# Optimization experiments

Measured on AMD Instinct MI355X. Metric: run time of the kernel, lower is better.

Reference implementation:

```python
import jax, jax.numpy as jnp
import numpy as np

EPS = 1e-5

def layer_norm(x, gamma, beta):
    mu = jnp.mean(x, axis=-1, keepdims=True)
    var = jnp.mean(jnp.square(x - mu), axis=-1, keepdims=True)
    return (x - mu) * jax.lax.rsqrt(var + EPS) * gamma + beta

def setup_inputs() -> dict:
    key = jax.random.key(0)
    ks = jax.random.split(key, 16)
    B, Cq, Hq, Wq = 8, 256, 32, 32
    Cc, Hc, Wc = 512, 64, 64
    def lin(k, fan_in, fan_out):
        lim = 1.0 / np.sqrt(fan_in)
        k1, k2 = jax.random.split(k)
        W = jax.random.uniform(k1, (fan_in, fan_out), jnp.float32, -lim, lim)
        b = jax.random.uniform(k2, (fan_out,), jnp.float32, -lim, lim)
        return W, b
    Wq_, bq = lin(ks[0], Cq, Cq)
    Wk_, bk = lin(ks[1], Cc, Cq)
    Wv_, bv = lin(ks[2], Cc, Cq)
    Wo_, bo = lin(ks[3], Cq, Cq)
    return {
        "query": jax.random.normal(ks[4], (B, Cq, Hq, Wq), jnp.float32),
        "context": jax.random.normal(ks[5], (B, Cc, Hc, Wc), jnp.float32),
        "Wq": Wq_, "bq": bq, "Wk": Wk_, "bk": bk, "Wv": Wv_, "bv": bv,
        "Wo": Wo_, "bo": bo,
        "gq": jnp.ones((Cq,), jnp.float32), "betq": jnp.zeros((Cq,), jnp.float32),
        "gc": jnp.ones((Cc,), jnp.float32), "betc": jnp.zeros((Cc,), jnp.float32),
    }

def reference(query, context, Wq, bq, Wk, bk, Wv, bv, Wo, bo, gq, betq, gc, betc):
    B, Cq, Hq, Wq_sp = query.shape
    _, Cc, Hc, Wc = context.shape
    num_heads = 8
    head_dim = Cq // num_heads
    scale = jnp.sqrt(jnp.float32(head_dim))
    N = Hq * Wq_sp
    # adaptive_avg_pool2d with divisible sizes == average pooling over equal bins
    ctx = context.reshape(B, Cc, Hq, Hc // Hq, Wq_sp, Wc // Wq_sp).mean(axis=(3, 5))
    q_flat = query.reshape(B, Cq, N).transpose(0, 2, 1)          # (B,N,Cq)
    c_flat = ctx.reshape(B, Cc, N).transpose(0, 2, 1)            # (B,N,Cc)
    qn = layer_norm(q_flat, gq, betq)
    cn = layer_norm(c_flat, gc, betc)
    q = (qn @ Wq + bq).reshape(B, N, num_heads, head_dim).transpose(0, 2, 1, 3)
    k = (cn @ Wk + bk).reshape(B, N, num_heads, head_dim).transpose(0, 2, 1, 3)
    v = (cn @ Wv + bv).reshape(B, N, num_heads, head_dim).transpose(0, 2, 1, 3)
    attn = jnp.einsum('bhnd,bhmd->bhnm', q, k) / scale
    attn = jax.nn.softmax(attn, axis=-1)
    out = jnp.einsum('bhnm,bhmd->bhnd', attn, v)
    out = out.transpose(0, 2, 1, 3).reshape(B, N, Cq)
    out = out @ Wo + bo
    out = q_flat + out                                           # residual
    return out.transpose(0, 2, 1).reshape(B, Cq, Hq, Wq_sp)
```

## Files before the change

### kernel.cpp

```cpp
#include <hip/hip_runtime.h>
#include <hip/hip_bf16.h>
#include <cstddef>

#define B_  8
#define CQ  256
#define CC  512
#define N_  1024
#define HQ  32
#define WQ  32
#define NH  8
#define HD  32

typedef __bf16 bf16x8 __attribute__((ext_vector_type(8)));
typedef float f32x4 __attribute__((ext_vector_type(4)));
typedef float f32x16 __attribute__((ext_vector_type(16)));
typedef unsigned int uint4v __attribute__((ext_vector_type(4)));
typedef unsigned short ushort8 __attribute__((ext_vector_type(8)));
typedef unsigned short ushort4v __attribute__((ext_vector_type(4)));

__device__ __forceinline__ unsigned short f2bf(float x) {
    return __builtin_bit_cast(unsigned short, __float2bfloat16(x));
}
__device__ __forceinline__ float bf2f(unsigned short x) {
    return __bfloat162float(__builtin_bit_cast(__hip_bfloat16, x));
}
__device__ __forceinline__ bf16x8 ldb8(const unsigned short* p) {
    return __builtin_bit_cast(bf16x8, *(const ushort8*)p);
}

__global__ __launch_bounds__(256) void prep_k(
    const float* __restrict__ query, const float* __restrict__ context,
    const float* __restrict__ Wq, const float* __restrict__ Wk,
    const float* __restrict__ Wv, const float* __restrict__ Wo,
    const float* __restrict__ gq, const float* __restrict__ betq,
    const float* __restrict__ gc, const float* __restrict__ betc,
    __hip_bfloat16* __restrict__ Wqt, __hip_bfloat16* __restrict__ Wkt,
    __hip_bfloat16* __restrict__ Wvt, __hip_bfloat16* __restrict__ Wot,
    __hip_bfloat16* __restrict__ qn, __hip_bfloat16* __restrict__ cn,
    __hip_bfloat16* __restrict__ qraw) {
    __shared__ float T[32][33];
    __shared__ float SsA[32][16];
    __shared__ float S2A[32][16];
    __shared__ float SsB[32][32];
    __shared__ float S2B[32][32];
    __shared__ float Mu[32], Rs[32];

    const int bid = blockIdx.x;
    const int tid = threadIdx.x;

    if (bid < 256) {
        const int nt = bid & 31, b = bid >> 5;
        const int nq = tid & 7;
        const int cg = tid >> 3;
        const int ch0 = cg * 8;
        const int nb  = nt * 32 + 4 * nq;

        const float* Qb = query + ((size_t)b * CQ + ch0) * N_ + nb;
        float qv[32];
        float ps[4] = {0.f, 0.f, 0.f, 0.f};
        float p2[4] = {0.f, 0.f, 0.f, 0.f};
        #pragma unroll
        for (int i = 0; i < 8; ++i) {
            const float4 v = *(const float4*)(Qb + (size_t)i * N_);
            qv[4 * i + 0] = v.x; qv[4 * i + 1] = v.y;
            qv[4 * i + 2] = v.z; qv[4 * i + 3] = v.w;
            ps[0] += v.x; p2[0] += v.x * v.x;
            ps[1] += v.y; p2[1] += v.y * v.y;
            ps[2] += v.z; p2[2] += v.z * v.z;
            ps[3] += v.w; p2[3] += v.w * v.w;
        }
        #pragma unroll
        for (int i = 0; i < 8; ++i) {
            ushort4v o;
            o[0] = f2bf(qv[4 * i + 0]); o[1] = f2bf(qv[4 * i + 1]);
            o[2] = f2bf(qv[4 * i + 2]); o[3] = f2bf(qv[4 * i + 3]);
            *(ushort4v*)((unsigned short*)qraw + ((size_t)b * CQ + ch0 + i) * N_ + nb) = o;
        }
        #pragma unroll
        for (int j = 0; j < 4; ++j) {
            SsB[cg][4 * nq + j] = ps[j];
            S2B[cg][4 * nq + j] = p2[j];
        }
        __syncthreads();
        if (tid < 32) {
            float ts = 0.f, t2 = 0.f;
            #pragma unroll
            for (int i = 0; i < 32; ++i) { ts += SsB[i][tid]; t2 += S2B[i][tid]; }
            const float mu  = ts * (1.f / CQ);
            const float var = t2 * (1.f / CQ) - mu * mu;
            Mu[tid] = mu; Rs[tid] = rsqrtf(var + 1e-5f);
        }
        __syncthreads();
        #pragma unroll
        for (int j = 0; j < 4; ++j) {
            const float mu = Mu[4 * nq + j], rs = Rs[4 * nq + j];
            ushort8 o;
            #pragma unroll
            for (int i = 0; i < 8; ++i)
                o[i] = f2bf((qv[4 * i + j] - mu) * rs * gq[ch0 + i] + betq[ch0 + i]);
            *(ushort8*)((unsigned short*)qn + ((size_t)b * N_ + nb + j) * CQ + ch0) = o;
        }
    } else if (bid < 768) {
        const int u    = bid - 256;
        const int wqc2 = u & 1, hq = (u >> 1) & 31, b = u >> 6;
        const int pp   = tid & 7;
        const int cg   = tid >> 3;
        const int ch0  = cg * 16;

        const float* Cb = context + ((size_t)b * CC + ch0) * 4096
                        + (size_t)(2 * hq) * 64 + (32 * wqc2 + 4 * pp);
        float pv0[16], pv1[16];
        float ss0 = 0.f, ss1 = 0.f, s20 = 0.f, s21 = 0.f;
        #pragma unroll
        for (int i = 0; i < 16; ++i) {
            const float4 r0 = *(const float4*)(Cb + (size_t)i * 4096);
            const float4 r1 = *(const float4*)(Cb + (size_t)i * 4096 + 64);
            const float v0 = (r0.x + r0.y + r1.x + r1.y) * 0.25f;
            const float v1 = (r0.z + r0.w + r1.z + r1.w) * 0.25f;
            pv0[i] = v0; pv1[i] = v1;
            ss0 += v0; s20 += v0 * v0;
            ss1 += v1; s21 += v1 * v1;
        }
        SsA[cg][2 * pp]     = ss0; S2A[cg][2 * pp]     = s20;
        SsA[cg][2 * pp + 1] = ss1; S2A[cg][2 * pp + 1] = s21;
        __syncthreads();
        if (tid < 16) {
            float ts = 0.f, t2 = 0.f;
            #pragma unroll
            for (int i = 0; i < 32; ++i) { ts += SsA[i][tid]; t2 += S2A[i][tid]; }
            const float mu  = ts * (1.f / CC);
            const float var = t2 * (1.f / CC) - mu * mu;
            Mu[tid] = mu; Rs[tid] = rsqrtf(var + 1e-5f);
        }
        __syncthreads();
        const float mu0 = Mu[2 * pp],     rs0 = Rs[2 * pp];
        const float mu1 = Mu[2 * pp + 1], rs1 = Rs[2 * pp + 1];
        const int pos0 = hq * 32 + wqc2 * 16 + 2 * pp;
        unsigned short* dst = (unsigned short*)cn
            + ((size_t)b * N_ + pos0) * CC + ch0;
        ushort8 a0, a1, b0, b1;
        #pragma unroll
        for (int i = 0; i < 8; ++i) {
            a0[i] = f2bf((pv0[i] - mu0) * rs0 * gc[ch0 + i] + betc[ch0 + i]);
            b0[i] = f2bf((pv1[i] - mu1) * rs1 * gc[ch0 + i] + betc[ch0 + i]);
        }
        #pragma unroll
        for (int i = 0; i < 8; ++i) {
            a1[i] = f2bf((pv0[8 + i] - mu0) * rs0 * gc[ch0 + 8 + i] + betc[ch0 + 8 + i]);
            b1[i] = f2bf((pv1[8 + i] - mu1) * rs1 * gc[ch0 + 8 + i] + betc[ch0 + 8 + i]);
        }
        *(ushort8*)(dst)          = a0;
        *(ushort8*)(dst + 8)      = a1;
        *(ushort8*)(dst + CC)     = b0;
        *(ushort8*)(dst + CC + 8) = b1;
    } else {
        const int u = bid - 768;
        const int x = u & 15, y = (u >> 4) & 7, z = u >> 7;
        const float* W; __hip_bfloat16* Wt; int K;
        switch (z) {
            case 0: W = Wq; Wt = Wqt; K = CQ; break;
            case 1: W = Wk; Wt = Wkt; K = CC; break;
            case 2: W = Wv; Wt = Wvt; K = CC; break;
            default: W = Wo; Wt = Wot; K = CQ; break;
        }
        const int k0 = x * 32;
        if (k0 >= K) return;
        const int c0 = y * 32;
        const int tx = tid & 31, ty = tid >> 5;
        #pragma unroll
        for (int i = 0; i < 4; ++i) {
            const int r = ty + 8 * i;
            T[r][tx] = W[(size_t)(k0 + r) * CQ + c0 + tx];
        }
        __syncthreads();
        #pragma unroll
        for (int i = 0; i < 4; ++i) {
            const int r = ty + 8 * i;
            Wt[(size_t)(c0 + r) * K + k0 + tx] = __float2bfloat16(T[tx][r]);
        }
    }
}

__global__ __launch_bounds__(256) void proj_all_k(
    const __hip_bfloat16* __restrict__ qn, const __hip_bfloat16* __restrict__ cn,
    const __hip_bfloat16* __restrict__ Wqt, const __hip_bfloat16* __restrict__ Wkt,
    const __hip_bfloat16* __restrict__ Wvt,
    const float* __restrict__ bq, const float* __restrict__ bk,
    const float* __restrict__ bv,
    __hip_bfloat16* __restrict__ Qb, __hip_bfloat16* __restrict__ Kb,
    __hip_bfloat16* __restrict__ Vt, float qsc) {
    __shared__ unsigned short As[64][40];
    __shared__ unsigned short B1[64][40];
    __shared__ unsigned short B2[64][40];

    const int zz = blockIdx.z;
    const int n0 = blockIdx.x * 64;
    const int c0 = blockIdx.y * 64;
    const int tid = threadIdx.x;
    const int wid = tid >> 6, lane = tid & 63;
    const int lg = lane >> 4, ln = lane & 15;
    const int wn0 = (wid & 1) * 32, wc0 = (wid >> 1) * 32;
    const int sr = tid >> 2;
    const int sk = (tid & 3) * 8;

    if (zz >= 8) {
        const int b = zz - 8;
        const unsigned short* Ab = (const unsigned short*)qn + ((size_t)b * N_ + n0) * CQ;
        const unsigned short* Wb = (const unsigned short*)Wqt + (size_t)c0 * CQ;
        f32x4 acc[2][2] = {};
        ushort8 ra = *(const ushort8*)(Ab + (size_t)sr * CQ + sk);
        ushort8 rw = *(const ushort8*)(Wb + (size_t)sr * CQ + sk);
        for (int t = 0; t < 8; ++t) {
            *(ushort8*)&As[sr][sk] = ra;
            *(ushort8*)&B1[sr][sk] = rw;
            __syncthreads();
            if (t < 7) {
                ra = *(const ushort8*)(Ab + (size_t)sr * CQ + (t + 1) * 32 + sk);
                rw = *(const ushort8*)(Wb + (size_t)sr * CQ + (t + 1) * 32 + sk);
            }
            bf16x8 a[2], w[2];
            #pragma unroll
            for (int i = 0; i < 2; ++i) a[i] = ldb8(&As[wn0 + 16 * i + ln][8 * lg]);
            #pragma unroll
            for (int j = 0; j < 2; ++j) w[j] = ldb8(&B1[wc0 + 16 * j + ln][8 * lg]);
            #pragma unroll
            for (int i = 0; i < 2; ++i)
                #pragma unroll
                for (int j = 0; j < 2; ++j)
                    acc[i][j] = __builtin_amdgcn_mfma_f32_16x16x32_bf16(a[i], w[j], acc[i][j], 0, 0, 0);
            __syncthreads();
        }
        #pragma unroll
        for (int j = 0; j < 2; ++j) {
            const int co = c0 + wc0 + 16 * j + ln;
            const int h = co >> 5, d = co & 31;
            const float bb = bq[co];
            #pragma unroll
            for (int i = 0; i < 2; ++i)
                #pragma unroll
                for (int r = 0; r < 4; ++r) {
                    const int n = n0 + wn0 + 16 * i + 4 * lg + r;
                    Qb[(((size_t)b * NH + h) * N_ + n) * HD + d] =
                        __float2bfloat16((acc[i][j][r] + bb) * qsc);
                }
        }
    } else {
        const int b = zz;
        const unsigned short* Ab  = (const unsigned short*)cn + ((size_t)b * N_ + n0) * CC;
        const unsigned short* Wkb = (const unsigned short*)Wkt + (size_t)c0 * CC;
        const unsigned short* Wvb = (const unsigned short*)Wvt + (size_t)c0 * CC;
        f32x4 accK[2][2] = {};
        f32x4 accV[2][2] = {};
        ushort8 ra = *(const ushort8*)(Ab  + (size_t)sr * CC + sk);
        ushort8 rk = *(const ushort8*)(Wkb + (size_t)sr * CC + sk);
        ushort8 rv = *(const ushort8*)(Wvb + (size_t)sr * CC + sk);
        for (int t = 0; t < 16; ++t) {
            *(ushort8*)&As[sr][sk] = ra;
            *(ushort8*)&B1[sr][sk] = rk;
            *(ushort8*)&B2[sr][sk] = rv;
            __syncthreads();
            if (t < 15) {
                ra = *(const ushort8*)(Ab  + (size_t)sr * CC + (t + 1) * 32 + sk);
                rk = *(const ushort8*)(Wkb + (size_t)sr * CC + (t + 1) * 32 + sk);
                rv = *(const ushort8*)(Wvb + (size_t)sr * CC + (t + 1) * 32 + sk);
            }
            bf16x8 a[2], wk[2], wv[2];
            #pragma unroll
            for (int i = 0; i < 2; ++i) {
                a[i]  = ldb8(&As[wn0 + 16 * i + ln][8 * lg]);
                wk[i] = ldb8(&B1[wc0 + 16 * i + ln][8 * lg]);
                wv[i] = ldb8(&B2[wc0 + 16 * i + ln][8 * lg]);
            }
            #pragma unroll
            for (int i = 0; i < 2; ++i)
                #pragma unroll
                for (int j = 0; j < 2; ++j) {
                    accK[i][j] = __builtin_amdgcn_mfma_f32_16x16x32_bf16(a[i], wk[j], accK[i][j], 0, 0, 0);
                    accV[i][j] = __builtin_amdgcn_mfma_f32_16x16x32_bf16(a[i], wv[j], accV[i][j], 0, 0, 0);
                }
            __syncthreads();
        }
        #pragma unroll
        for (int j = 0; j < 2; ++j) {
            const int co = c0 + wc0 + 16 * j + ln;
            const int h = co >> 5, d = co & 31;
            const float bbk = bk[co], bbv = bv[co];
            #pragma unroll
            for (int i = 0; i < 2; ++i) {
                const int nb = n0 + wn0 + 16 * i + 4 * lg;
                #pragma unroll
                for (int r = 0; r < 4; ++r)
                    Kb[(((size_t)b * NH + h) * N_ + nb + r) * HD + d] =
                        __float2bfloat16(accK[i][j][r] + bbk);
                ushort4v o;
                #pragma unroll
                for (int r = 0; r < 4; ++r) o[r] = f2bf(accV[i][j][r] + bbv);
                const int g  = (nb >> 2) & 3;
                const int gp = ((g & 1) << 1) | (g >> 1);
                const int nbp = (nb & ~15) | (gp << 2);
                *(ushort4v*)((unsigned short*)Vt + (((size_t)b * NH + h) * HD + d) * N_ + nbp) = o;
            }
        }
    }
}

__global__ __launch_bounds__(256) void attn32_k(
    const __hip_bfloat16* __restrict__ Q,
    const __hip_bfloat16* __restrict__ K,
    const __hip_bfloat16* __restrict__ Vt,
    __hip_bfloat16* __restrict__ O) {
    __shared__ float accS[2][64][20];
    __shared__ float lwS[2][64];

    const int lin = blockIdx.x + 16 * blockIdx.y;
    const int eff = (lin & 7) * 128 + (lin >> 3);
    const int qt  = eff & 15;
    const int bh  = eff >> 4;
    const int b   = bh >> 3;
    const int h   = bh & 7;
    const int wid  = threadIdx.x >> 6;
    const int lane = threadIdx.x & 63;
    const int l31  = lane & 31;
    const int hh   = lane >> 5;
    const int qsub = wid >> 1;
    const int kvh  = wid & 1;
    const int q0   = qt * 64 + qsub * 32;

    const unsigned short* Qp = (const unsigned short*)Q + ((size_t)bh * N_ + q0) * HD;
    const unsigned short* Kbb = (const unsigned short*)K + (size_t)bh * N_ * HD;
    const unsigned short* Vb = (const unsigned short*)Vt + ((size_t)bh * HD + l31) * N_;

    bf16x8 qB[2];
    #pragma unroll
    for (int m = 0; m < 2; ++m)
        qB[m] = ldb8(Qp + (size_t)l31 * HD + 16 * m + 8 * hh);

    const f32x16 Z = {0.f,0.f,0.f,0.f,0.f,0.f,0.f,0.f,
                      0.f,0.f,0.f,0.f,0.f,0.f,0.f,0.f};
    f32x16 acc = Z;
    float ls0 = 0.f, ls1 = 0.f, ls2 = 0.f, ls3 = 0.f;

    const int kvbase = kvh * 512;
    const unsigned short* kp = Kbb + (size_t)(kvbase + l31) * HD + 8 * hh;
    const unsigned short* vp = Vb + kvbase + 8 * hh;

    bf16x8 kaA[2][4];
    #pragma unroll
    for (int j = 0; j < 4; ++j)
        kaA[0][j] = ldb8(kp + (j >> 1) * 1024 + (j & 1) * 16);

    #pragma unroll
    for (int st = 0; st < 8; ++st) {
        const int cur = st & 1;
        bf16x8 va[4];
        #pragma unroll
        for (int j = 0; j < 4; ++j)
            va[j] = ldb8(vp + st * 64 + 16 * j);
        if (st < 7) {
            const unsigned short* kp2 = kp + (size_t)(st + 1) * 2048;
            #pragma unroll
            for (int j = 0; j < 4; ++j)
                kaA[cur ^ 1][j] = ldb8(kp2 + (j >> 1) * 1024 + (j & 1) * 16);
        }

        f32x16 s0, s1;
        s0 = __builtin_amdgcn_mfma_f32_32x32x16_bf16(kaA[cur][0], qB[0], Z, 0, 0, 0);
        s0 = __builtin_amdgcn_mfma_f32_32x32x16_bf16(kaA[cur][1], qB[1], s0, 0, 0, 0);
        s1 = __builtin_amdgcn_mfma_f32_32x32x16_bf16(kaA[cur][2], qB[0], Z, 0, 0, 0);
        s1 = __builtin_amdgcn_mfma_f32_32x32x16_bf16(kaA[cur][3], qB[1], s1, 0, 0, 0);

        unsigned int pk[2][4][2];
        #pragma unroll
        for (int T = 0; T < 2; ++T) {
            float p[16];
            #pragma unroll
            for (int r = 0; r < 16; ++r)
                p[r] = __builtin_amdgcn_exp2f(T == 0 ? s0[r] : s1[r]);
            #pragma unroll
            for (int r = 0; r < 16; r += 4) {
                ls0 += p[r]; ls1 += p[r + 1]; ls2 += p[r + 2]; ls3 += p[r + 3];
            }
            #pragma unroll
            for (int c = 0; c < 4; ++c) {
                asm("v_cvt_pk_bf16_f32 %0, %1, %2"
                    : "=v"(pk[T][c][0]) : "v"(p[4 * c]), "v"(p[4 * c + 1]));
                asm("v_cvt_pk_bf16_f32 %0, %1, %2"
                    : "=v"(pk[T][c][1]) : "v"(p[4 * c + 2]), "v"(p[4 * c + 3]));
            }
        }

        #pragma unroll
        for (int w = 0; w < 4; ++w) {
            const int T = w >> 1, cp = w & 1;
            uint4v fu = {pk[T][2 * cp][0], pk[T][2 * cp][1],
                         pk[T][2 * cp + 1][0], pk[T][2 * cp + 1][1]};
            const bf16x8 pa = __builtin_bit_cast(bf16x8, fu);
            acc = __builtin_amdgcn_mfma_f32_32x32x16_bf16(pa, va[w], acc, 0, 0, 0);
        }
    }

    const float lsum = (ls0 + ls1) + (ls2 + ls3);
    const float lw = lsum + __shfl_xor(lsum, 32);

    if (kvh == 1) {
        #pragma unroll
        for (int r4 = 0; r4 < 4; ++r4) {
            float4 v = {acc[4 * r4], acc[4 * r4 + 1], acc[4 * r4 + 2], acc[4 * r4 + 3]};
            *(float4*)&accS[qsub][lane][4 * r4] = v;
        }
        lwS[qsub][lane] = lw;
    }
    __syncthreads();
    if (kvh == 0) {
        const float linv = 1.0f / (lw + lwS[qsub][lane]);
        #pragma unroll
        for (int r = 0; r < 16; ++r) {
            const int ql = (r & 3) + 8 * (r >> 2) + 4 * hh;
            const float vv = (acc[r] + accS[qsub][lane][r]) * __shfl(linv, ql);
            O[((size_t)b * N_ + q0 + ql) * CQ + h * HD + l31] = __float2bfloat16(vv);
        }
    }
}

__global__ __launch_bounds__(256) void out_proj_k(const __hip_bfloat16* __restrict__ Ob,
                              const __hip_bfloat16* __restrict__ Wot,
                              const float* __restrict__ bo,
                              const __hip_bfloat16* __restrict__ qraw,
                              float* __restrict__ out) {
    __shared__ unsigned short As[64][40];
    __shared__ unsigned short Bs[64][40];
    const int b  = blockIdx.z;
    const int n0 = blockIdx.x * 64;
    const int c0 = blockIdx.y * 64;
    const int tid = threadIdx.x;
    const int wid = tid >> 6, lane = tid & 63;
    const int lg = lane >> 4, ln = lane & 15;
    const int wn0 = (wid & 1) * 32, wc0 = (wid >> 1) * 32;

    const unsigned short* Ab = (const unsigned short*)Ob + ((size_t)b * N_ + n0) * CQ;
    const unsigned short* Wb = (const unsigned short*)Wot + (size_t)c0 * CQ;
    const int sr = tid >> 2;
    const int sk = (tid & 3) * 8;

    f32x4 acc[2][2] = {};
    ushort8 ra = *(const ushort8*)(Ab + (size_t)sr * CQ + sk);
    ushort8 rw = *(const ushort8*)(Wb + (size_t)sr * CQ + sk);

    for (int t = 0; t < 8; ++t) {
        *(ushort8*)&As[sr][sk] = ra;
        *(ushort8*)&Bs[sr][sk] = rw;
        __syncthreads();
        if (t < 7) {
            ra = *(const ushort8*)(Ab + (size_t)sr * CQ + (t + 1) * 32 + sk);
            rw = *(const ushort8*)(Wb + (size_t)sr * CQ + (t + 1) * 32 + sk);
        }
        bf16x8 a[2], w[2];
        #pragma unroll
        for (int i = 0; i < 2; ++i)
            a[i] = ldb8(&As[wn0 + 16 * i + ln][8 * lg]);
        #pragma unroll
        for (int j = 0; j < 2; ++j)
            w[j] = ldb8(&Bs[wc0 + 16 * j + ln][8 * lg]);
        #pragma unroll
        for (int i = 0; i < 2; ++i)
            #pragma unroll
            for (int j = 0; j < 2; ++j)
                acc[i][j] = __builtin_amdgcn_mfma_f32_16x16x32_bf16(a[i], w[j], acc[i][j], 0, 0, 0);
        __syncthreads();
    }

    #pragma unroll
    for (int j = 0; j < 2; ++j) {
        const int co = c0 + wc0 + 16 * j + ln;
        const float bb = bo[co];
        #pragma unroll
        for (int i = 0; i < 2; ++i) {
            const int nb = n0 + wn0 + 16 * i + 4 * lg;
            const ushort4v res = *(const ushort4v*)((const unsigned short*)qraw
                + ((size_t)b * CQ + co) * N_ + nb);
            float4 o;
            o.x = acc[i][j][0] + bb + bf2f(res[0]);
            o.y = acc[i][j][1] + bb + bf2f(res[1]);
            o.z = acc[i][j][2] + bb + bf2f(res[2]);
            o.w = acc[i][j][3] + bb + bf2f(res[3]);
            *(float4*)&out[((size_t)b * CQ + co) * N_ + nb] = o;
        }
    }
}

extern "C" void kernel_launch(void* const* d_in, const int* in_sizes, int n_in,
                              void* d_out, int out_size, void* d_ws, size_t ws_size,
                              hipStream_t stream) {
    const float* query   = (const float*)d_in[0];
    const float* context = (const float*)d_in[1];
    const float* Wq = (const float*)d_in[2];
    const float* bq = (const float*)d_in[3];
    const float* Wk = (const float*)d_in[4];
    const float* bk = (const float*)d_in[5];
    const float* Wv = (const float*)d_in[6];
    const float* bv = (const float*)d_in[7];
    const float* Wo = (const float*)d_in[8];
    const float* bo = (const float*)d_in[9];
    const float* gq   = (const float*)d_in[10];
    const float* betq = (const float*)d_in[11];
    const float* gc   = (const float*)d_in[12];
    const float* betc = (const float*)d_in[13];
    float* out = (float*)d_out;

    char* w = (char*)d_ws;
    __hip_bfloat16* qn   = (__hip_bfloat16*)w;  w += (size_t)B_ * N_ * CQ * 2;
    __hip_bfloat16* cn   = (__hip_bfloat16*)w;  w += (size_t)B_ * N_ * CC * 2;
    __hip_bfloat16* qraw = (__hip_bfloat16*)w;  w += (size_t)B_ * CQ * N_ * 2;
    __hip_bfloat16* Qb   = (__hip_bfloat16*)w;  w += (size_t)B_ * NH * N_ * HD * 2;
    __hip_bfloat16* Kb   = (__hip_bfloat16*)w;  w += (size_t)B_ * NH * N_ * HD * 2;
    __hip_bfloat16* Vt   = (__hip_bfloat16*)w;  w += (size_t)B_ * NH * HD * N_ * 2;
    __hip_bfloat16* Ob   = (__hip_bfloat16*)w;  w += (size_t)B_ * N_ * CQ * 2;
    __hip_bfloat16* Wqt  = (__hip_bfloat16*)w;  w += (size_t)CQ * CQ * 2;
    __hip_bfloat16* Wkt  = (__hip_bfloat16*)w;  w += (size_t)CQ * CC * 2;
    __hip_bfloat16* Wvt  = (__hip_bfloat16*)w;  w += (size_t)CQ * CC * 2;
    __hip_bfloat16* Wot  = (__hip_bfloat16*)w;  w += (size_t)CQ * CQ * 2;

    prep_k<<<dim3(1280), 256, 0, stream>>>(query, context, Wq, Wk, Wv, Wo,
                                           gq, betq, gc, betc,
                                           Wqt, Wkt, Wvt, Wot, qn, cn, qraw);

    const float qsc = 0.17677669529663687f * 1.4426950408889634f;
    proj_all_k<<<dim3(16, 4, 16), 256, 0, stream>>>(qn, cn, Wqt, Wkt, Wvt,
                                                    bq, bk, bv, Qb, Kb, Vt, qsc);

    attn32_k<<<dim3(16, 64), 256, 0, stream>>>(Qb, Kb, Vt, Ob);

    out_proj_k<<<dim3(16, 4, 8), 256, 0, stream>>>(Ob, Wot, bo, qraw, out);
}
```

Baseline: 66.62 us.

## Fuse attention and output projection into one kernel with all heads per block

Merges the attention kernel and the output-projection GEMM into a single kernel. Each 1024-thread block now handles 32 queries across all 8 heads (two KV halves per head). The normalized attention output is staged in LDS as bf16, then multiplied by Wo, with bias and residual added in the same kernel. This removes the Ob round trip through global memory and one launch. In exchange the grid shrinks to 256 large blocks, which may lower occupancy, and every block reloads Wo from global/L2.

```diff
diff --git a/kernel.cpp b/kernel.cpp
--- a/kernel.cpp
+++ b/kernel.cpp
@@ -304,31 +304,34 @@
     }
 }
 
-__global__ __launch_bounds__(256) void attn32_k(
+__global__ __launch_bounds__(1024) void attn_out_k(
     const __hip_bfloat16* __restrict__ Q,
     const __hip_bfloat16* __restrict__ K,
     const __hip_bfloat16* __restrict__ Vt,
-    __hip_bfloat16* __restrict__ O) {
-    __shared__ float accS[2][64][20];
-    __shared__ float lwS[2][64];
-
-    const int lin = blockIdx.x + 16 * blockIdx.y;
-    const int eff = (lin & 7) * 128 + (lin >> 3);
-    const int qt  = eff & 15;
-    const int bh  = eff >> 4;
-    const int b   = bh >> 3;
-    const int h   = bh & 7;
+    const __hip_bfloat16* __restrict__ Wot,
+    const float* __restrict__ bo,
+    const __hip_bfloat16* __restrict__ qraw,
+    float* __restrict__ out) {
+    __shared__ float accS[8][64][20];
+    __shared__ float lwS[8][64];
+    __shared__ unsigned short ObL[32][264];
+
+    const int lin = blockIdx.x;
+    const int eff = (lin & 7) * 32 + (lin >> 3);
+    const int qt  = eff & 31;
+    const int b   = eff >> 5;
     const int wid  = threadIdx.x >> 6;
     const int lane = threadIdx.x & 63;
     const int l31  = lane & 31;
     const int hh   = lane >> 5;
-    const int qsub = wid >> 1;
-    const int kvh  = wid & 1;
-    const int q0   = qt * 64 + qsub * 32;
-
-    const unsigned short* Qp = (const unsigned short*)Q + ((size_t)bh * N_ + q0) * HD;
+    const int h    = wid & 7;
+    const int kvh  = wid >> 3;
+    const int q0   = qt * 32;
+    const int bh   = b * NH + h;
+
+    const unsigned short* Qp  = (const unsigned short*)Q + ((size_t)bh * N_ + q0) * HD;
     const unsigned short* Kbb = (const unsigned short*)K + (size_t)bh * N_ * HD;
-    const unsigned short* Vb = (const unsigned short*)Vt + ((size_t)bh * HD + l31) * N_;
+    const unsigned short* Vb  = (const unsigned short*)Vt + ((size_t)bh * HD + l31) * N_;
 
     bf16x8 qB[2];
     #pragma unroll
@@ -406,85 +409,51 @@
         #pragma unroll
         for (int r4 = 0; r4 < 4; ++r4) {
             float4 v = {acc[4 * r4], acc[4 * r4 + 1], acc[4 * r4 + 2], acc[4 * r4 + 3]};
-            *(float4*)&accS[qsub][lane][4 * r4] = v;
-        }
-        lwS[qsub][lane] = lw;
+            *(float4*)&accS[h][lane][4 * r4] = v;
+        }
+        lwS[h][lane] = lw;
     }
     __syncthreads();
     if (kvh == 0) {
-        const float linv = 1.0f / (lw + lwS[qsub][lane]);
+        const float linv = 1.0f / (lw + lwS[h][lane]);
         #pragma unroll
         for (int r = 0; r < 16; ++r) {
             const int ql = (r & 3) + 8 * (r >> 2) + 4 * hh;
-            const float vv = (acc[r] + accS[qsub][lane][r]) * __shfl(linv, ql);
-            O[((size_t)b * N_ + q0 + ql) * CQ + h * HD + l31] = __float2bfloat16(vv);
-        }
-    }
-}
-
-__global__ __launch_bounds__(256) void out_proj_k(const __hip_bfloat16* __restrict__ Ob,
-                              const __hip_bfloat16* __restrict__ Wot,
-                              const float* __restrict__ bo,
-                              const __hip_bfloat16* __restrict__ qraw,
-                              float* __restrict__ out) {
-    __shared__ unsigned short As[64][40];
-    __shared__ unsigned short Bs[64][40];
-    const int b  = blockIdx.z;
-    const int n0 = blockIdx.x * 64;
-    const int c0 = blockIdx.y * 64;
-    const int tid = threadIdx.x;
-    const int wid = tid >> 6, lane = tid & 63;
+            const float vv = (acc[r] + accS[h][lane][r]) * __shfl(linv, ql);
+            ObL[ql][h * HD + l31] = f2bf(vv);
+        }
+    }
+    __syncthreads();
+
     const int lg = lane >> 4, ln = lane & 15;
-    const int wn0 = (wid & 1) * 32, wc0 = (wid >> 1) * 32;
-
-    const unsigned short* Ab = (const unsigned short*)Ob + ((size_t)b * N_ + n0) * CQ;
-    const unsigned short* Wb = (const unsigned short*)Wot + (size_t)c0 * CQ;
-    const int sr = tid >> 2;
-    const int sk = (tid & 3) * 8;
-
-    f32x4 acc[2][2] = {};
-    ushort8 ra = *(const ushort8*)(Ab + (size_t)sr * CQ + sk);
-    ushort8 rw = *(const ushort8*)(Wb + (size_t)sr * CQ + sk);
-
+    const int co0 = wid * 16;
+    const unsigned short* Wb = (const unsigned short*)Wot + (size_t)co0 * CQ;
+
+    f32x4 acc2[2] = {};
+    #pragma unroll
     for (int t = 0; t < 8; ++t) {
-        *(ushort8*)&As[sr][sk] = ra;
-        *(ushort8*)&Bs[sr][sk] = rw;
-        __syncthreads();
-        if (t < 7) {
-            ra = *(const ushort8*)(Ab + (size_t)sr * CQ + (t + 1) * 32 + sk);
-            rw = *(const ushort8*)(Wb + (size_t)sr * CQ + (t + 1) * 32 + sk);
-        }
-        bf16x8 a[2], w[2];
-        #pragma unroll
-        for (int i = 0; i < 2; ++i)
-            a[i] = ldb8(&As[wn0 + 16 * i + ln][8 * lg]);
-        #pragma unroll
-        for (int j = 0; j < 2; ++j)
-            w[j] = ldb8(&Bs[wc0 + 16 * j + ln][8 * lg]);
-        #pragma unroll
-        for (int i = 0; i < 2; ++i)
-            #pragma unroll
-            for (int j = 0; j < 2; ++j)
-                acc[i][j] = __builtin_amdgcn_mfma_f32_16x16x32_bf16(a[i], w[j], acc[i][j], 0, 0, 0);
-        __syncthreads();
-    }
-
+        const int k0 = t * 32;
+        const bf16x8 w = ldb8(Wb + (size_t)ln * CQ + k0 + 8 * lg);
+        #pragma unroll
+        for (int i = 0; i < 2; ++i) {
+            const bf16x8 a = ldb8(&ObL[16 * i + ln][k0 + 8 * lg]);
+            acc2[i] = __builtin_amdgcn_mfma_f32_16x16x32_bf16(a, w, acc2[i], 0, 0, 0);
+        }
+    }
+
+    const int co = co0 + ln;
+    const float bb = bo[co];
     #pragma unroll
-    for (int j = 0; j < 2; ++j) {
-        const int co = c0 + wc0 + 16 * j + ln;
-        const float bb = bo[co];
-        #pragma unroll
-        for (int i = 0; i < 2; ++i) {
-            const int nb = n0 + wn0 + 16 * i + 4 * lg;
-            const ushort4v res = *(const ushort4v*)((const unsigned short*)qraw
-                + ((size_t)b * CQ + co) * N_ + nb);
-            float4 o;
-            o.x = acc[i][j][0] + bb + bf2f(res[0]);
-            o.y = acc[i][j][1] + bb + bf2f(res[1]);
-            o.z = acc[i][j][2] + bb + bf2f(res[2]);
-            o.w = acc[i][j][3] + bb + bf2f(res[3]);
-            *(float4*)&out[((size_t)b * CQ + co) * N_ + nb] = o;
-        }
+    for (int i = 0; i < 2; ++i) {
+        const int nb = q0 + 16 * i + 4 * lg;
+        const ushort4v res = *(const ushort4v*)((const unsigned short*)qraw
+            + ((size_t)b * CQ + co) * N_ + nb);
+        float4 o;
+        o.x = acc2[i][0] + bb + bf2f(res[0]);
+        o.y = acc2[i][1] + bb + bf2f(res[1]);
+        o.z = acc2[i][2] + bb + bf2f(res[2]);
+        o.w = acc2[i][3] + bb + bf2f(res[3]);
+        *(float4*)&out[((size_t)b * CQ + co) * N_ + nb] = o;
     }
 }
 
@@ -514,7 +483,6 @@
     __hip_bfloat16* Qb   = (__hip_bfloat16*)w;  w += (size_t)B_ * NH * N_ * HD * 2;
     __hip_bfloat16* Kb   = (__hip_bfloat16*)w;  w += (size_t)B_ * NH * N_ * HD * 2;
     __hip_bfloat16* Vt   = (__hip_bfloat16*)w;  w += (size_t)B_ * NH * HD * N_ * 2;
-    __hip_bfloat16* Ob   = (__hip_bfloat16*)w;  w += (size_t)B_ * N_ * CQ * 2;
     __hip_bfloat16* Wqt  = (__hip_bfloat16*)w;  w += (size_t)CQ * CQ * 2;
     __hip_bfloat16* Wkt  = (__hip_bfloat16*)w;  w += (size_t)CQ * CC * 2;
     __hip_bfloat16* Wvt  = (__hip_bfloat16*)w;  w += (size_t)CQ * CC * 2;
@@ -528,7 +496,5 @@
     proj_all_k<<<dim3(16, 4, 16), 256, 0, stream>>>(qn, cn, Wqt, Wkt, Wvt,
                                                     bq, bk, bv, Qb, Kb, Vt, qsc);
 
-    attn32_k<<<dim3(16, 64), 256, 0, stream>>>(Qb, Kb, Vt, Ob);
-
-    out_proj_k<<<dim3(16, 4, 8), 256, 0, stream>>>(Ob, Wot, bo, qraw, out);
-}
+    attn_out_k<<<dim3(256), 1024, 0, stream>>>(Qb, Kb, Vt, Wot, bo, qraw, out);
+}
```

Measured after the change: 64.70 us (median of 2 runs). -2.9%, faster.
